# Kernel optimization log

Hardware: AMD Instinct MI355X
Metric: run time of the kernel (lower is better)

Reference implementation:

```python
import jax, jax.numpy as jnp
import numpy as np

N_NODES = 100000
N_EDGES = 1600000
D = 64
L = 4
D_TGT = 32


def setup_inputs() -> dict:
    key = jax.random.key(0)
    ks = jax.random.split(key, 8)
    x = jax.random.normal(ks[0], (N_NODES, D), dtype=jnp.float32)
    edge_index = jax.random.randint(ks[1], (2, N_EDGES), 0, N_NODES, dtype=jnp.int64)
    s = 1.0 / np.sqrt(D)
    Wl = jax.random.normal(ks[2], (L, D, D), dtype=jnp.float32) * s
    bl = jnp.zeros((L, D), dtype=jnp.float32)
    Wr = jax.random.normal(ks[3], (L, D, D), dtype=jnp.float32) * s
    Wp = jax.random.normal(ks[4], (L * D, D_TGT), dtype=jnp.float32) * (1.0 / np.sqrt(L * D))
    bp = jnp.zeros((D_TGT,), dtype=jnp.float32)
    return {"x": x, "edge_index": edge_index, "Wl": Wl, "bl": bl, "Wr": Wr, "Wp": Wp, "bp": bp}


def reference(x, edge_index, Wl, bl, Wr, Wp, bp):
    src, dst = edge_index[0], edge_index[1]
    n = x.shape[0]
    # in-degree per node, clamped to avoid div-by-zero (PyG mean gives 0 for isolated nodes;
    # sum is 0 there so clamping matches)
    deg = jax.ops.segment_sum(jnp.ones_like(dst, dtype=x.dtype), dst, num_segments=n)
    deg = jnp.maximum(deg, 1.0)[:, None]
    h = x
    outs = []
    for i in range(Wl.shape[0]):
        # SAGEConv: out = lin_l(mean_{j in N(i)} h_j) + lin_r(h_i)
        agg = jax.ops.segment_sum(h[src], dst, num_segments=n) / deg
        h = agg @ Wl[i] + bl[i] + h @ Wr[i]
        outs.append(h)
    h_cat = jnp.concatenate(outs, axis=1)  # [N, L*D]
    return h_cat @ Wp + bp  # [N, D_TGT]
```

## Files before the change

kernel.cpp:

```cpp
#include <hip/hip_runtime.h>
#include <hip/hip_fp16.h>

#define NN 100000
#define NE 1600000
#define NNP (NN + 64)

#define NPB 512
#define NBUK ((NN + NPB - 1) / NPB)
#define EPB 2048
#define ABLK ((NE + EPB - 1) / EPB)
#define BCAP 10240

typedef _Float16 half8 __attribute__((ext_vector_type(8)));
typedef float f32x4 __attribute__((ext_vector_type(4)));


__global__ __launch_bounds__(256) void bucket_init(int* __restrict__ bucket_cur) {
  int t = blockIdx.x * 256 + threadIdx.x;
  if (t < NBUK) bucket_cur[t] = t * BCAP;
}

__global__ __launch_bounds__(256) void binA(const int* __restrict__ src,
                                            const int* __restrict__ dst,
                                            int* __restrict__ bucket_cur,
                                            unsigned* __restrict__ binned) {
  __shared__ int hist[NBUK];
  __shared__ int sc[256];
  __shared__ int lbase[NBUK];
  __shared__ int gbase[NBUK];
  __shared__ int lcur[NBUK];
  __shared__ uint2 stage[EPB];
  int t = threadIdx.x;
  int e0 = blockIdx.x * EPB;
  if (t < NBUK) hist[t] = 0;
  __syncthreads();
  int es[8], ed[8];
#pragma unroll
  for (int j = 0; j < 8; ++j) {
    int e = e0 + t + j * 256;
    if (e < NE) {
      es[j] = src[e];
      ed[j] = dst[e];
      atomicAdd(&hist[ed[j] >> 9], 1);
    } else {
      es[j] = -1;
      ed[j] = 0;
    }
  }
  __syncthreads();
  sc[t] = (t < NBUK) ? hist[t] : 0;
  __syncthreads();
  for (int off = 1; off < 256; off <<= 1) {
    int v = (t >= off) ? sc[t - off] : 0;
    __syncthreads();
    sc[t] += v;
    __syncthreads();
  }
  if (t < NBUK) {
    int h = hist[t];
    int lb = sc[t] - h;
    lbase[t] = lb;
    lcur[t] = lb;
    if (h > 0) gbase[t] = atomicAdd(&bucket_cur[t], h);
  }
  __syncthreads();
#pragma unroll
  for (int j = 0; j < 8; ++j) {
    if (es[j] >= 0) {
      int b = ed[j] >> 9;
      int slot = atomicAdd(&lcur[b], 1);
      stage[slot] = make_uint2((unsigned)es[j], (unsigned)ed[j]);
    }
  }
  __syncthreads();
  int total = min(EPB, NE - e0);
  for (int i = t; i < total; i += 256) {
    uint2 p = stage[i];
    int b = (int)(p.y >> 9);
    binned[(size_t)gbase[b] + (i - lbase[b])] = (p.x << 9) | (p.y & 511u);
  }
}

__global__ __launch_bounds__(256) void bucket_scan(const int* __restrict__ bucket_cur,
                                                   int* __restrict__ bucket_base,
                                                   int* __restrict__ row_ptr) {
  __shared__ int part[256];
  int t = threadIdx.x;
  int v = (t < NBUK) ? (bucket_cur[t] - t * BCAP) : 0;
  part[t] = v;
  __syncthreads();
  for (int off = 1; off < 256; off <<= 1) {
    int u = (t >= off) ? part[t - off] : 0;
    __syncthreads();
    part[t] += u;
    __syncthreads();
  }
  if (t < NBUK) bucket_base[t] = part[t] - v;
  if (t == 0) row_ptr[NN] = NE;
}

__global__ __launch_bounds__(256) void binB(const unsigned* __restrict__ binned,
                                            const int* __restrict__ bucket_cur,
                                            const int* __restrict__ bucket_base,
                                            int* __restrict__ row_ptr,
                                            float* __restrict__ deg_inv,
                                            int* __restrict__ col) {
  __shared__ int hist[NPB];
  __shared__ int cur2[NPB];
  __shared__ int part[256];
  __shared__ int srcS[BCAP];
  int b = blockIdx.x;
  int n0 = b * NPB;
  int n1 = min(n0 + NPB, NN);
  int cnt = bucket_cur[b] - b * BCAP;
  int gb = bucket_base[b];
  size_t seg = (size_t)b * BCAP;
  int t = threadIdx.x;
  hist[t] = 0;
  hist[t + 256] = 0;
  __syncthreads();
  for (int i = t; i < cnt; i += 256)
    atomicAdd(&hist[(int)(binned[seg + i] & 511u)], 1);
  __syncthreads();
  int c0 = hist[2 * t], c1 = hist[2 * t + 1];
  int s = c0 + c1;
  part[t] = s;
  __syncthreads();
  for (int off = 1; off < 256; off <<= 1) {
    int u = (t >= off) ? part[t - off] : 0;
    __syncthreads();
    part[t] += u;
    __syncthreads();
  }
  int excl = part[t] - s;
  cur2[2 * t] = excl;
  cur2[2 * t + 1] = excl + c0;
  int n = n0 + 2 * t;
  if (n < n1) {
    row_ptr[n] = gb + excl;
    deg_inv[n] = 1.0f / (float)(c0 > 1 ? c0 : 1);
  }
  if (n + 1 < n1) {
    row_ptr[n + 1] = gb + excl + c0;
    deg_inv[n + 1] = 1.0f / (float)(c1 > 1 ? c1 : 1);
  }
  __syncthreads();
  for (int i = t; i < cnt; i += 256) {
    unsigned p = binned[seg + i];
    int slot = atomicAdd(&cur2[(int)(p & 511u)], 1);
    srcS[slot] = (int)(p >> 9);
  }
  __syncthreads();
  for (int i = t; i < cnt; i += 256) col[(size_t)gb + i] = srcS[i];
}


__global__ __launch_bounds__(256) void tohalf(const float* __restrict__ x,
                                              __half* __restrict__ x16) {
  size_t o = ((size_t)blockIdx.x * 256 + threadIdx.x) * 8;
  float4 a = *(const float4*)(x + o);
  float4 b = *(const float4*)(x + o + 4);
  union { uint4 u; __half h[8]; } U;
  U.h[0] = __float2half(a.x); U.h[1] = __float2half(a.y);
  U.h[2] = __float2half(a.z); U.h[3] = __float2half(a.w);
  U.h[4] = __float2half(b.x); U.h[5] = __float2half(b.y);
  U.h[6] = __float2half(b.z); U.h[7] = __float2half(b.w);
  *(uint4*)(x16 + o) = U.u;
}


__global__ __launch_bounds__(256) void prep_weights(const float* __restrict__ Wl,
                                                    const float* __restrict__ Wr,
                                                    const float* __restrict__ Wp,
                                                    _Float16* __restrict__ WcatT,
                                                    _Float16* __restrict__ WpT) {
  int t = blockIdx.x * 256 + threadIdx.x;
  if (t < 4 * 64 * 128) {
    int l = t >> 13, rem = t & 8191, j = rem >> 7, k = rem & 127;
    float v = (k < 64) ? Wl[l * 4096 + k * 64 + j] : Wr[l * 4096 + (k - 64) * 64 + j];
    WcatT[t] = (_Float16)v;
  }
  if (t < 4 * 32 * 64) {
    int l = t >> 11, rem = t & 2047, j = rem >> 6, k = rem & 63;
    WpT[t] = (_Float16)Wp[(size_t)(l * 64 + k) * 32 + j];
  }
}


#define PADA 72
#define PADC 72

__global__ __launch_bounds__(256, 4) void fused_layer(
    const _Float16* __restrict__ h16,
    const int* __restrict__ row_ptr, const int* __restrict__ col,
    const float* __restrict__ deginv,
    const _Float16* __restrict__ WcatT, const float* __restrict__ bl,
    const _Float16* __restrict__ WpT, const float* __restrict__ bp,
    _Float16* __restrict__ hn16, float* __restrict__ out, int flags) {
  __shared__ _Float16 aggS[64 * PADA];
  __shared__ _Float16 cS[64 * PADC];
  int tid = threadIdx.x;
  int w = tid >> 6, l = tid & 63;
  int base = blockIdx.x * 64;

  for (int i = 0; i < 16; ++i) {
    int n = base + (w << 4) + i;
    float acc = 0.f;
    if (n < NN) {
      int beg = row_ptr[n], end = row_ptr[n + 1];
      int e = beg;
      while (e < end) {
        int chunk = end - e;
        if (chunk > 64) chunk = 64;
        int cv = col[e + (l < chunk ? l : chunk - 1)];
        int q = 0;
        for (; q + 8 <= chunk; q += 8) {
          int s0 = __shfl(cv, q + 0, 64), s1 = __shfl(cv, q + 1, 64);
          int s2 = __shfl(cv, q + 2, 64), s3 = __shfl(cv, q + 3, 64);
          int s4 = __shfl(cv, q + 4, 64), s5 = __shfl(cv, q + 5, 64);
          int s6 = __shfl(cv, q + 6, 64), s7 = __shfl(cv, q + 7, 64);
          float v0 = (float)h16[(size_t)s0 * 64 + l];
          float v1 = (float)h16[(size_t)s1 * 64 + l];
          float v2 = (float)h16[(size_t)s2 * 64 + l];
          float v3 = (float)h16[(size_t)s3 * 64 + l];
          float v4 = (float)h16[(size_t)s4 * 64 + l];
          float v5 = (float)h16[(size_t)s5 * 64 + l];
          float v6 = (float)h16[(size_t)s6 * 64 + l];
          float v7 = (float)h16[(size_t)s7 * 64 + l];
          acc += ((v0 + v1) + (v2 + v3)) + ((v4 + v5) + (v6 + v7));
        }
        for (; q < chunk; ++q) {
          int s = __shfl(cv, q, 64);
          acc += (float)h16[(size_t)s * 64 + l];
        }
        e += chunk;
      }
      acc *= deginv[n];
    }
    aggS[((w << 4) + i) * PADA + l] = (_Float16)acc;
  }
  __syncthreads();

  int lr = l & 15, lg = l >> 4;
  int arow = base + (w << 4) + lr;

  f32x4 acc4[4];
#pragma unroll
  for (int ct = 0; ct < 4; ++ct) {
    float b = bl[ct * 16 + lr];
    acc4[ct] = (f32x4){b, b, b, b};
  }
  const half8 a0 = *(const half8*)(aggS + ((w << 4) + lr) * PADA + lg * 8);
  const half8 a1 = *(const half8*)(aggS + ((w << 4) + lr) * PADA + 32 + lg * 8);
  const half8 a2 = *(const half8*)(h16 + (size_t)arow * 64 + lg * 8);
  const half8 a3 = *(const half8*)(h16 + (size_t)arow * 64 + 32 + lg * 8);
#pragma unroll
  for (int ct = 0; ct < 4; ++ct) {
    const _Float16* wb = WcatT + (ct * 16 + lr) * 128 + lg * 8;
    half8 b0 = *(const half8*)(wb);
    half8 b1 = *(const half8*)(wb + 32);
    half8 b2 = *(const half8*)(wb + 64);
    half8 b3 = *(const half8*)(wb + 96);
    acc4[ct] = __builtin_amdgcn_mfma_f32_16x16x32_f16(a0, b0, acc4[ct], 0, 0, 0);
    acc4[ct] = __builtin_amdgcn_mfma_f32_16x16x32_f16(a1, b1, acc4[ct], 0, 0, 0);
    acc4[ct] = __builtin_amdgcn_mfma_f32_16x16x32_f16(a2, b2, acc4[ct], 0, 0, 0);
    acc4[ct] = __builtin_amdgcn_mfma_f32_16x16x32_f16(a3, b3, acc4[ct], 0, 0, 0);
  }

#pragma unroll
  for (int ct = 0; ct < 4; ++ct)
#pragma unroll
    for (int r = 0; r < 4; ++r)
      cS[((w << 4) + (lg << 2) + r) * PADC + ct * 16 + lr] = (_Float16)acc4[ct][r];
  __syncthreads();

  if (flags & 2) {
#pragma unroll
    for (int j = 0; j < 2; ++j) {
      int idx = tid + j * 256;
      int row = idx >> 3, c8 = (idx & 7) * 8;
      *(half8*)(hn16 + (size_t)(base + row) * 64 + c8) =
          *(const half8*)(cS + row * PADC + c8);
    }
  }

  f32x4 pacc[2];
#pragma unroll
  for (int pt = 0; pt < 2; ++pt) {
    int colo = pt * 16 + lr;
    if (flags & 1) {
      float b = bp[colo];
      pacc[pt] = (f32x4){b, b, b, b};
    } else {
#pragma unroll
      for (int r = 0; r < 4; ++r) {
        int row = base + (w << 4) + (lg << 2) + r;
        pacc[pt][r] = (row < NN) ? out[(size_t)row * 32 + colo] : 0.f;
      }
    }
  }
  const _Float16* crow = cS + ((w << 4) + lr) * PADC + lg * 8;
  half8 c0 = *(const half8*)(crow);
  half8 c1 = *(const half8*)(crow + 32);
#pragma unroll
  for (int pt = 0; pt < 2; ++pt) {
    const _Float16* wp = WpT + (pt * 16 + lr) * 64 + lg * 8;
    half8 w0 = *(const half8*)(wp);
    half8 w1 = *(const half8*)(wp + 32);
    pacc[pt] = __builtin_amdgcn_mfma_f32_16x16x32_f16(c0, w0, pacc[pt], 0, 0, 0);
    pacc[pt] = __builtin_amdgcn_mfma_f32_16x16x32_f16(c1, w1, pacc[pt], 0, 0, 0);
  }
#pragma unroll
  for (int pt = 0; pt < 2; ++pt) {
    int colo = pt * 16 + lr;
#pragma unroll
    for (int r = 0; r < 4; ++r) {
      int row = base + (w << 4) + (lg << 2) + r;
      if (row < NN) out[(size_t)row * 32 + colo] = pacc[pt][r];
    }
  }
}


extern "C" void kernel_launch(void* const* d_in, const int* in_sizes, int n_in,
                              void* d_out, int out_size, void* d_ws, size_t ws_size,
                              hipStream_t stream) {
  const float* x  = (const float*)d_in[0];
  const int*   ei = (const int*)d_in[1];
  const float* Wl = (const float*)d_in[2];
  const float* bl = (const float*)d_in[3];
  const float* Wr = (const float*)d_in[4];
  const float* Wp = (const float*)d_in[5];
  const float* bp = (const float*)d_in[6];
  float* out = (float*)d_out;

  char* ws = (char*)d_ws;
  size_t off = 0;
  auto alloc = [&](size_t bytes) {
    void* p = ws + off;
    off = (off + bytes + 255) & ~(size_t)255;
    return p;
  };
  int*      row_ptr     = (int*)alloc(((size_t)NN + 1) * 4);
  float*    deginv      = (float*)alloc((size_t)NN * 4);
  int*      col         = (int*)alloc((size_t)NE * 4);
  int*      bucket_cur  = (int*)alloc((size_t)NBUK * 4);
  int*      bucket_base = (int*)alloc((size_t)NBUK * 4);
  unsigned* binned      = (unsigned*)alloc((size_t)NBUK * BCAP * 4);
  __half*   x16         = (__half*)alloc((size_t)NNP * 64 * 2);
  __half*   h16A        = (__half*)alloc((size_t)NNP * 64 * 2);
  __half*   h16B        = (__half*)alloc((size_t)NNP * 64 * 2);
  _Float16* WcatT       = (_Float16*)alloc((size_t)4 * 64 * 128 * 2);
  _Float16* WpT         = (_Float16*)alloc((size_t)4 * 32 * 64 * 2);

  tohalf<<<3125, 256, 0, stream>>>(x, x16);
  prep_weights<<<128, 256, 0, stream>>>(Wl, Wr, Wp, WcatT, WpT);
  bucket_init<<<1, 256, 0, stream>>>(bucket_cur);
  binA<<<ABLK, 256, 0, stream>>>(ei, ei + NE, bucket_cur, binned);
  bucket_scan<<<1, 256, 0, stream>>>(bucket_cur, bucket_base, row_ptr);
  binB<<<NBUK, 256, 0, stream>>>(binned, bucket_cur, bucket_base, row_ptr, deginv, col);

  const __half* cur16 = x16;
  __half* bufs[2] = {h16A, h16B};
  int nblk = (NN + 63) / 64;
  for (int l = 0; l < 4; ++l) {
    __half* nxt = bufs[l & 1];
    int flags = (l == 0 ? 1 : 0) | (l < 3 ? 2 : 0);
    fused_layer<<<nblk, 256, 0, stream>>>(
        (const _Float16*)cur16, row_ptr, col, deginv,
        WcatT + l * 8192, bl + l * 64, WpT + l * 2048, bp,
        (_Float16*)nxt, out, flags);
    cur16 = nxt;
  }
}
```

Baseline: 419.2 us.

## Vectorize neighbor gather: 4 edges per wavefront step, two nodes interleaved

Restructures the aggregation loop so each lane loads 4 fp16 features (8 bytes) per neighbor, letting a 64-lane wave cover four neighbor rows at once. Two destination nodes are processed together to raise memory-level parallelism. Partial sums are combined with cross-lane xor shuffles. Edges beyond 64 per node go through a slow serial fallback, and the change adds shuffle/reduction overhead and predication.

```diff
diff --git a/kernel.cpp b/kernel.cpp
--- a/kernel.cpp
+++ b/kernel.cpp
@@ -190,6 +190,14 @@
 #define PADA 72
 #define PADC 72
 
+#define ACC4(acc, v)                                        \
+  {                                                         \
+    float2 _a = __half22float2(*(__half2*)&(v).x);          \
+    float2 _b = __half22float2(*(__half2*)&(v).y);          \
+    (acc)[0] += _a.x; (acc)[1] += _a.y;                     \
+    (acc)[2] += _b.x; (acc)[3] += _b.y;                     \
+  }
+
 __global__ __launch_bounds__(256, 4) void fused_layer(
     const _Float16* __restrict__ h16,
     const int* __restrict__ row_ptr, const int* __restrict__ col,
@@ -202,42 +210,82 @@
   int tid = threadIdx.x;
   int w = tid >> 6, l = tid & 63;
   int base = blockIdx.x * 64;
-
-  for (int i = 0; i < 16; ++i) {
-    int n = base + (w << 4) + i;
-    float acc = 0.f;
-    if (n < NN) {
-      int beg = row_ptr[n], end = row_ptr[n + 1];
-      int e = beg;
-      while (e < end) {
-        int chunk = end - e;
-        if (chunk > 64) chunk = 64;
-        int cv = col[e + (l < chunk ? l : chunk - 1)];
-        int q = 0;
-        for (; q + 8 <= chunk; q += 8) {
-          int s0 = __shfl(cv, q + 0, 64), s1 = __shfl(cv, q + 1, 64);
-          int s2 = __shfl(cv, q + 2, 64), s3 = __shfl(cv, q + 3, 64);
-          int s4 = __shfl(cv, q + 4, 64), s5 = __shfl(cv, q + 5, 64);
-          int s6 = __shfl(cv, q + 6, 64), s7 = __shfl(cv, q + 7, 64);
-          float v0 = (float)h16[(size_t)s0 * 64 + l];
-          float v1 = (float)h16[(size_t)s1 * 64 + l];
-          float v2 = (float)h16[(size_t)s2 * 64 + l];
-          float v3 = (float)h16[(size_t)s3 * 64 + l];
-          float v4 = (float)h16[(size_t)s4 * 64 + l];
-          float v5 = (float)h16[(size_t)s5 * 64 + l];
-          float v6 = (float)h16[(size_t)s6 * 64 + l];
-          float v7 = (float)h16[(size_t)s7 * 64 + l];
-          acc += ((v0 + v1) + (v2 + v3)) + ((v4 + v5) + (v6 + v7));
-        }
-        for (; q < chunk; ++q) {
-          int s = __shfl(cv, q, 64);
-          acc += (float)h16[(size_t)s * 64 + l];
-        }
-        e += chunk;
+  int r4 = l >> 4;
+  int fq = (l & 15) * 4;
+
+  for (int i = 0; i < 8; ++i) {
+    int nA = base + (w << 4) + 2 * i;
+    int nB = nA + 1;
+    int ia = min(nA, NN), ib = min(nB, NN), ic = min(nB + 1, NN);
+    int begA = row_ptr[ia];
+    int mid  = row_ptr[ib];
+    int endB = row_ptr[ic];
+    int chAt = mid - begA;
+    int chBt = endB - mid;
+    int chA = min(chAt, 64), chB = min(chBt, 64);
+    f32x4 accA = (f32x4){0.f, 0.f, 0.f, 0.f};
+    f32x4 accB = (f32x4){0.f, 0.f, 0.f, 0.f};
+    int cvA = 0, cvB = 0;
+    if (chA > 0) cvA = col[begA + (l < chA ? l : chA - 1)];
+    if (chB > 0) cvB = col[mid + (l < chB ? l : chB - 1)];
+    int gA = (chA + 3) >> 2, gB = (chB + 3) >> 2;
+    int gm = gA > gB ? gA : gB;
+    int g = 0;
+    for (; g + 2 <= gm; g += 2) {
+      bool fa0 = g < gA, fb0 = g < gB, fa1 = g + 1 < gA, fb1 = g + 1 < gB;
+      int q0 = 4 * g + r4, q1 = q0 + 4;
+      uint2 va0, vb0, va1, vb1;
+      if (fa0) va0 = *(const uint2*)(h16 + (size_t)__shfl(cvA, q0 < chA ? q0 : chA - 1, 64) * 64 + fq);
+      if (fb0) vb0 = *(const uint2*)(h16 + (size_t)__shfl(cvB, q0 < chB ? q0 : chB - 1, 64) * 64 + fq);
+      if (fa1) va1 = *(const uint2*)(h16 + (size_t)__shfl(cvA, q1 < chA ? q1 : chA - 1, 64) * 64 + fq);
+      if (fb1) vb1 = *(const uint2*)(h16 + (size_t)__shfl(cvB, q1 < chB ? q1 : chB - 1, 64) * 64 + fq);
+      if (fa0 && q0 < chA) ACC4(accA, va0);
+      if (fb0 && q0 < chB) ACC4(accB, vb0);
+      if (fa1 && q1 < chA) ACC4(accA, va1);
+      if (fb1 && q1 < chB) ACC4(accB, vb1);
+    }
+    if (g < gm) {
+      bool fa = g < gA, fb = g < gB;
+      int q0 = 4 * g + r4;
+      uint2 va, vb;
+      if (fa) va = *(const uint2*)(h16 + (size_t)__shfl(cvA, q0 < chA ? q0 : chA - 1, 64) * 64 + fq);
+      if (fb) vb = *(const uint2*)(h16 + (size_t)__shfl(cvB, q0 < chB ? q0 : chB - 1, 64) * 64 + fq);
+      if (fa && q0 < chA) ACC4(accA, va);
+      if (fb && q0 < chB) ACC4(accB, vb);
+    }
+    if (__builtin_expect(chAt > 64, 0)) {
+      for (int e = begA + 64; e < mid; ++e) {
+        uint2 v = *(const uint2*)(h16 + (size_t)col[e] * 64 + fq);
+        if (r4 == 0) ACC4(accA, v);
       }
-      acc *= deginv[n];
-    }
-    aggS[((w << 4) + i) * PADA + l] = (_Float16)acc;
+    }
+    if (__builtin_expect(chBt > 64, 0)) {
+      for (int e = mid + 64; e < endB; ++e) {
+        uint2 v = *(const uint2*)(h16 + (size_t)col[e] * 64 + fq);
+        if (r4 == 0) ACC4(accB, v);
+      }
+    }
+#pragma unroll
+    for (int k = 0; k < 4; ++k) {
+      accA[k] += __shfl_xor(accA[k], 16, 64);
+      accB[k] += __shfl_xor(accB[k], 16, 64);
+      accA[k] += __shfl_xor(accA[k], 32, 64);
+      accB[k] += __shfl_xor(accB[k], 32, 64);
+    }
+    int rowA = (w << 4) + 2 * i;
+    if (l < 16) {
+      float di = (nA < NN) ? deginv[nA] : 0.f;
+      union { uint2 u; __half2 h2[2]; } P;
+      P.h2[0] = __floats2half2_rn(accA[0] * di, accA[1] * di);
+      P.h2[1] = __floats2half2_rn(accA[2] * di, accA[3] * di);
+      *(uint2*)(aggS + rowA * PADA + (l & 15) * 4) = P.u;
+    } else if (l < 32) {
+      float di = (nB < NN) ? deginv[nB] : 0.f;
+      union { uint2 u; __half2 h2[2]; } P;
+      P.h2[0] = __floats2half2_rn(accB[0] * di, accB[1] * di);
+      P.h2[1] = __floats2half2_rn(accB[2] * di, accB[3] * di);
+      *(uint2*)(aggS + (rowA + 1) * PADA + (l & 15) * 4) = P.u;
+    }
   }
   __syncthreads();
 
```

New measurement: 393.3 us. 6.2% less time.
